# Kernel optimization log

Measured on AMD Instinct MI355X. Metric: run time of the kernel, lower is better.

## Reference

```python
import jax, jax.numpy as jnp
import numpy as np

DIM = 2048
HQ = 32
HKV = 8
HD = DIM // HQ  # 64
B, T = 2, 2048


def _rope_tables(key_unused):
    # Standard RoPE tables: cos/sin of shape [B, T, HD]
    inv_freq = 1.0 / (10000.0 ** (np.arange(0, HD, 2, dtype=np.float32) / HD))
    t = np.arange(T, dtype=np.float32)
    freqs = np.outer(t, inv_freq)                 # [T, HD/2]
    emb = np.concatenate([freqs, freqs], axis=-1)  # [T, HD]
    cos = jnp.asarray(np.cos(emb))[None].repeat(B, axis=0)
    sin = jnp.asarray(np.sin(emb))[None].repeat(B, axis=0)
    return cos, sin


def setup_inputs() -> dict:
    key = jax.random.key(0)
    ks = jax.random.split(key, 8)
    s_in = 1.0 / np.sqrt(DIM)
    x = jax.random.normal(ks[0], (B, T, DIM), dtype=jnp.float32)
    cos, sin = _rope_tables(None)
    # Linear weights stored as [in, out] (transposed vs torch)
    Wq = jax.random.normal(ks[1], (DIM, HQ * HD), dtype=jnp.float32) * s_in
    bq = jnp.zeros((HQ * HD,), dtype=jnp.float32)
    Wk = jax.random.normal(ks[2], (DIM, HKV * HD), dtype=jnp.float32) * s_in
    bk = jnp.zeros((HKV * HD,), dtype=jnp.float32)
    Wv = jax.random.normal(ks[3], (DIM, HKV * HD), dtype=jnp.float32) * s_in
    bv = jnp.zeros((HKV * HD,), dtype=jnp.float32)
    Wo = jax.random.normal(ks[4], (HQ * HD, DIM), dtype=jnp.float32) * s_in
    return {"x": x, "cos": cos, "sin": sin, "Wq": Wq, "bq": bq,
            "Wk": Wk, "bk": bk, "Wv": Wv, "bv": bv, "Wo": Wo}


def _rotate_half(u):
    u1, u2 = jnp.split(u, 2, axis=-1)
    return jnp.concatenate([-u2, u1], axis=-1)


def reference(x, cos, sin, Wq, bq, Wk, bk, Wv, bv, Wo):
    Bx, Tx, D = x.shape
    g = HQ // HKV  # group size (queries per kv head)
    q = (x @ Wq + bq).reshape(Bx, Tx, HQ, HD).transpose(0, 2, 1, 3)   # [B,Hq,T,d]
    k = (x @ Wk + bk).reshape(Bx, Tx, HKV, HD).transpose(0, 2, 1, 3)  # [B,Hkv,T,d]
    v = (x @ Wv + bv).reshape(Bx, Tx, HKV, HD).transpose(0, 2, 1, 3)
    c = cos[:, None, :, :]  # [B,1,T,d]
    s = sin[:, None, :, :]
    q = q * c + _rotate_half(q) * s
    k = k * c + _rotate_half(k) * s
    # GQA: group query heads over shared KV heads instead of repeat_interleave
    qg = q.reshape(Bx, HKV, g, Tx, HD)
    scale = 1.0 / np.sqrt(HD)
    scores = jnp.einsum('bkgtd,bksd->bkgts', qg, k) * scale  # [B,Hkv,g,T,T]
    causal = jnp.tril(jnp.ones((Tx, Tx), dtype=bool))
    scores = jnp.where(causal, scores, jnp.finfo(scores.dtype).min)
    probs = jax.nn.softmax(scores, axis=-1)
    out = jnp.einsum('bkgts,bksd->bkgtd', probs, v)           # [B,Hkv,g,T,d]
    out = out.reshape(Bx, HQ, Tx, HD).transpose(0, 2, 1, 3).reshape(Bx, Tx, HQ * HD)
    return out @ Wo
```

## Files before the change

kernel.cpp:

```cpp
#include <hip/hip_runtime.h>


typedef short s8v __attribute__((ext_vector_type(8)));
typedef float f4v __attribute__((ext_vector_type(4)));

__device__ __forceinline__ unsigned short f2bf(float f) {
  unsigned int u = __float_as_uint(f);
  u += 0x7fffu + ((u >> 16) & 1u);
  return (unsigned short)(u >> 16);
}

__device__ __forceinline__ void llds16(const void* g, void* l) {
  __builtin_amdgcn_global_load_lds(
      (__attribute__((address_space(1))) void*)(g),
      (__attribute__((address_space(3))) void*)(l), 16, 0, 0);
}


__global__ __launch_bounds__(256) void cvt_bf16_k(const float* __restrict__ src,
                                                  unsigned short* __restrict__ dst, int n4) {
  int i = blockIdx.x * blockDim.x + threadIdx.x;
  if (i < n4) {
    float4 v = ((const float4*)src)[i];
    ushort4 o;
    o.x = f2bf(v.x); o.y = f2bf(v.y); o.z = f2bf(v.z); o.w = f2bf(v.w);
    ((ushort4*)dst)[i] = o;
  }
}

__global__ __launch_bounds__(256) void transpose_cvt(const float* __restrict__ src,
                                                     unsigned short* __restrict__ dst,
                                                     int srcW, int K) {
  __shared__ float tile[32][33];
  const int tx = threadIdx.x, ty = threadIdx.y;
  const int x = blockIdx.x * 32 + tx;
  const int ybase = blockIdx.y * 32;
#pragma unroll
  for (int j = 0; j < 32; j += 8)
    tile[ty + j][tx] = src[(size_t)(ybase + ty + j) * srcW + x];
  __syncthreads();
  const int x2 = ybase + tx;
  const int y2 = blockIdx.x * 32 + ty;
#pragma unroll
  for (int j = 0; j < 32; j += 8)
    dst[(size_t)(y2 + j) * K + x2] = f2bf(tile[tx][ty + j]);
}

__device__ __forceinline__ void gemm128(const unsigned short* __restrict__ A,
                                        const unsigned short* __restrict__ Bt,
                                        int K, int m0, int n0,
                                        unsigned short* As, unsigned short* Bs,
                                        f4v acc[4][4]) {
  const int tid = threadIdx.x;
  const int lane = tid & 63;
  const int w = tid >> 6;
  const int wm = w >> 1, wn = w & 1;
  const int c = lane & 15, quad = lane >> 4;
  const int srow = tid >> 2, scol = (tid & 3) * 8;
  for (int k0 = 0; k0 < K; k0 += 32) {
    const unsigned short* ga = A + (size_t)(m0 + srow) * K + k0 + scol;
    const unsigned short* gb = Bt + (size_t)(n0 + srow) * K + k0 + scol;
    llds16(ga,          As + w * 512);
    llds16(ga + 64 * K, As + 2048 + w * 512);
    llds16(gb,          Bs + w * 512);
    llds16(gb + 64 * K, Bs + 2048 + w * 512);
    __syncthreads();
    s8v a[4], b[4];
#pragma unroll
    for (int i = 0; i < 4; ++i)
      a[i] = *(const s8v*)&As[(wm * 64 + i * 16 + c) * 32 + quad * 8];
#pragma unroll
    for (int i = 0; i < 4; ++i)
      b[i] = *(const s8v*)&Bs[(wn * 64 + i * 16 + c) * 32 + quad * 8];
#pragma unroll
    for (int mb = 0; mb < 4; ++mb)
#pragma unroll
      for (int nb = 0; nb < 4; ++nb)
        acc[mb][nb] = __builtin_amdgcn_mfma_f32_16x16x32_bf16(a[mb], b[nb], acc[mb][nb], 0, 0, 0);
    __syncthreads();
  }
}

__global__ __launch_bounds__(256) void gemm_qkv(const unsigned short* __restrict__ A,
    const unsigned short* __restrict__ Bt,
    const float* __restrict__ bq, const float* __restrict__ bk, const float* __restrict__ bv,
    const float* __restrict__ cosp, const float* __restrict__ sinp,
    unsigned short* __restrict__ Qb, unsigned short* __restrict__ Kb,
    unsigned short* __restrict__ Vt) {
  __shared__ unsigned short As[4096], Bs[4096];
  const f4v fzero = {0.f, 0.f, 0.f, 0.f};
  f4v acc[4][4];
#pragma unroll
  for (int i = 0; i < 4; ++i)
#pragma unroll
    for (int j = 0; j < 4; ++j) acc[i][j] = fzero;
  const int m0 = blockIdx.y * 128, n0 = blockIdx.x * 128;
  gemm128(A, Bt, 2048, m0, n0, As, Bs, acc);

  const int tid = threadIdx.x, lane = tid & 63, w = tid >> 6;
  const int wm = w >> 1, wn = w & 1, c = lane & 15, quad = lane >> 4;
  const int nbase = n0 + wn * 64;
#pragma unroll
  for (int mb = 0; mb < 4; ++mb) {
#pragma unroll
    for (int r = 0; r < 4; ++r) {
      const int row = m0 + wm * 64 + mb * 16 + quad * 4 + r;
      const int b = row >> 11, t = row & 2047;
      if (nbase < 2048) {
        const int h = nbase >> 6;
        const size_t ob = ((size_t)(b * 32 + h) * 2048 + t) * 64;
        const float* cb = cosp + (size_t)row * 64;
        const float* sb = sinp + (size_t)row * 64;
#pragma unroll
        for (int nb = 0; nb < 2; ++nb) {
          const int d0 = nb * 16 + c, d1 = d0 + 32;
          const float v0 = acc[mb][nb][r] + bq[nbase + d0];
          const float v1 = acc[mb][nb + 2][r] + bq[nbase + d1];
          Qb[ob + d0] = f2bf(v0 * cb[d0] - v1 * sb[d0]);
          Qb[ob + d1] = f2bf(v1 * cb[d1] + v0 * sb[d1]);
        }
      } else if (nbase < 2560) {
        const int h = (nbase - 2048) >> 6;
        const size_t ob = ((size_t)(b * 8 + h) * 2048 + t) * 64;
        const float* cb = cosp + (size_t)row * 64;
        const float* sb = sinp + (size_t)row * 64;
#pragma unroll
        for (int nb = 0; nb < 2; ++nb) {
          const int d0 = nb * 16 + c, d1 = d0 + 32;
          const float v0 = acc[mb][nb][r] + bk[nbase - 2048 + d0];
          const float v1 = acc[mb][nb + 2][r] + bk[nbase - 2048 + d1];
          Kb[ob + d0] = f2bf(v0 * cb[d0] - v1 * sb[d0]);
          Kb[ob + d1] = f2bf(v1 * cb[d1] + v0 * sb[d1]);
        }
      } else {
        const int h = (nbase - 2560) >> 6;
        const size_t vb = (size_t)(b * 8 + h) * 64;
        const int tl = t & 63;
        const int tp = (t & ~63) | (((tl & 15) << 2) | (tl >> 4));
#pragma unroll
        for (int nb = 0; nb < 4; ++nb) {
          const int d = nb * 16 + c;
          Vt[(vb + d) * 2048 + tp] = f2bf(acc[mb][nb][r] + bv[nbase - 2560 + d]);
        }
      }
    }
  }
}

__global__ __launch_bounds__(256) void attn_k(const unsigned short* __restrict__ Qb,
                                              const unsigned short* __restrict__ Kb,
                                              const unsigned short* __restrict__ Vt,
                                              unsigned short* __restrict__ An) {
  __shared__ unsigned short Qs[4096], Ks[4096], Vs[4096], Ps[4096];
  const int tid = threadIdx.x, lane = tid & 63, w = tid >> 6;
  const int c = lane & 15, quad = lane >> 4;
  const int bh = blockIdx.y;
  const int b = bh >> 5, h = bh & 31, kvh = h >> 2;
  const int qt = gridDim.x - 1 - blockIdx.x;
  const int q0 = qt * 64;
  const unsigned short* gQ = Qb + ((size_t)bh * 2048 + q0) * 64;
  const unsigned short* gK = Kb + (size_t)(b * 8 + kvh) * 2048 * 64;
  const unsigned short* gV = Vt + (size_t)(b * 8 + kvh) * 64 * 2048;

  const int r0 = tid >> 3;
  const int ch8 = (((tid & 7) ^ (r0 & 7))) * 8;

  llds16(gQ + r0 * 64 + ch8,        Qs + w * 512);
  llds16(gQ + (r0 + 32) * 64 + ch8, Qs + 2048 + w * 512);
  __syncthreads();

  const int xq0 = (quad ^ (c & 7)) * 8;
  const int xq1 = ((quad + 4) ^ (c & 7)) * 8;
  const s8v aq0 = *(const s8v*)&Qs[(w * 16 + c) * 64 + xq0];
  const s8v aq1 = *(const s8v*)&Qs[(w * 16 + c) * 64 + xq1];

  const f4v fzero = {0.f, 0.f, 0.f, 0.f};
  f4v O[4];
  float lrp[4];
#pragma unroll
  for (int i = 0; i < 4; ++i) { O[i] = fzero; lrp[i] = 0.f; }

  const float kscale = 0.125f * 1.44269504089f;
  const int ntiles = qt + 1;
  for (int it = 0; it < ntiles; ++it) {
    const int s0 = it * 64;
    llds16(gK + (size_t)(s0 + r0) * 64 + ch8,      Ks + w * 512);
    llds16(gK + (size_t)(s0 + r0 + 32) * 64 + ch8, Ks + 2048 + w * 512);
    llds16(gV + (size_t)r0 * 2048 + s0 + ch8,          Vs + w * 512);
    llds16(gV + (size_t)(r0 + 32) * 2048 + s0 + ch8,   Vs + 2048 + w * 512);
    __syncthreads();

    f4v S[4];
#pragma unroll
    for (int nb = 0; nb < 4; ++nb) {
      const s8v bk0 = *(const s8v*)&Ks[(nb * 16 + c) * 64 + xq0];
      const s8v bk1 = *(const s8v*)&Ks[(nb * 16 + c) * 64 + xq1];
      f4v z = fzero;
      z = __builtin_amdgcn_mfma_f32_16x16x32_bf16(aq0, bk0, z, 0, 0, 0);
      z = __builtin_amdgcn_mfma_f32_16x16x32_bf16(aq1, bk1, z, 0, 0, 0);
      S[nb] = z;
    }

    const bool diag = (it == qt);
#pragma unroll
    for (int r = 0; r < 4; ++r) {
      const int rloc = quad * 4 + r;
      float p[4];
#pragma unroll
      for (int nb = 0; nb < 4; ++nb) {
        float sv = S[nb][r] * kscale;
        if (diag && (nb * 16 + c > w * 16 + rloc)) sv = -1e30f;
        p[nb] = __builtin_amdgcn_exp2f(sv);
      }
      lrp[r] += (p[0] + p[1]) + (p[2] + p[3]);
      ushort4 pk;
      pk.x = f2bf(p[0]); pk.y = f2bf(p[1]); pk.z = f2bf(p[2]); pk.w = f2bf(p[3]);
      *(ushort4*)&Ps[w * 1024 + rloc * 64 + (((c >> 1) ^ (rloc & 7)) * 8) + (c & 1) * 4] = pk;
    }
    asm volatile("s_waitcnt lgkmcnt(0)" ::: "memory");

    const s8v ap0 = *(const s8v*)&Ps[w * 1024 + c * 64 + xq0];
    const s8v ap1 = *(const s8v*)&Ps[w * 1024 + c * 64 + xq1];
#pragma unroll
    for (int nbd = 0; nbd < 4; ++nbd) {
      const s8v bv0 = *(const s8v*)&Vs[(nbd * 16 + c) * 64 + xq0];
      const s8v bv1 = *(const s8v*)&Vs[(nbd * 16 + c) * 64 + xq1];
      O[nbd] = __builtin_amdgcn_mfma_f32_16x16x32_bf16(ap0, bv0, O[nbd], 0, 0, 0);
      O[nbd] = __builtin_amdgcn_mfma_f32_16x16x32_bf16(ap1, bv1, O[nbd], 0, 0, 0);
    }
    __syncthreads();
  }

#pragma unroll
  for (int r = 0; r < 4; ++r) {
    float ps = lrp[r];
    ps += __shfl_xor(ps, 1, 64);
    ps += __shfl_xor(ps, 2, 64);
    ps += __shfl_xor(ps, 4, 64);
    ps += __shfl_xor(ps, 8, 64);
    const float inv = 1.0f / ps;
    const int t = q0 + w * 16 + quad * 4 + r;
    const size_t rowb = ((size_t)b * 2048 + t) * 2048 + h * 64;
#pragma unroll
    for (int nbd = 0; nbd < 4; ++nbd)
      An[rowb + nbd * 16 + c] = f2bf(O[nbd][r] * inv);
  }
}

__global__ __launch_bounds__(256) void gemm_out(const unsigned short* __restrict__ A,
                                                const unsigned short* __restrict__ Bt,
                                                float* __restrict__ C) {
  __shared__ unsigned short As[4096], Bs[4096];
  const f4v fzero = {0.f, 0.f, 0.f, 0.f};
  f4v acc[4][4];
#pragma unroll
  for (int i = 0; i < 4; ++i)
#pragma unroll
    for (int j = 0; j < 4; ++j) acc[i][j] = fzero;
  const int m0 = blockIdx.y * 128, n0 = blockIdx.x * 128;
  gemm128(A, Bt, 2048, m0, n0, As, Bs, acc);
  const int tid = threadIdx.x, lane = tid & 63, w = tid >> 6;
  const int wm = w >> 1, wn = w & 1, c = lane & 15, quad = lane >> 4;
#pragma unroll
  for (int mb = 0; mb < 4; ++mb)
#pragma unroll
    for (int r = 0; r < 4; ++r) {
      const int row = m0 + wm * 64 + mb * 16 + quad * 4 + r;
#pragma unroll
      for (int nb = 0; nb < 4; ++nb)
        C[(size_t)row * 2048 + n0 + wn * 64 + nb * 16 + c] = acc[mb][nb][r];
    }
}

extern "C" void kernel_launch(void* const* d_in, const int* in_sizes, int n_in,
                              void* d_out, int out_size, void* d_ws, size_t ws_size,
                              hipStream_t stream) {
  const float* x    = (const float*)d_in[0];
  const float* cosp = (const float*)d_in[1];
  const float* sinp = (const float*)d_in[2];
  const float* Wq   = (const float*)d_in[3];
  const float* bq   = (const float*)d_in[4];
  const float* Wk   = (const float*)d_in[5];
  const float* bk   = (const float*)d_in[6];
  const float* Wv   = (const float*)d_in[7];
  const float* bv   = (const float*)d_in[8];
  const float* Wo   = (const float*)d_in[9];
  float* out = (float*)d_out;

  char* ws = (char*)d_ws;
  unsigned short* xb  = (unsigned short*)(ws);
  unsigned short* Wt  = (unsigned short*)(ws + 16777216);
  unsigned short* Wot = (unsigned short*)(ws + 29360128);
  unsigned short* Qb  = (unsigned short*)(ws + 37748736);
  unsigned short* Kb  = (unsigned short*)(ws + 54525952);
  unsigned short* Vt  = (unsigned short*)(ws + 58720256);
  unsigned short* An  = (unsigned short*)(ws + 62914560);

  cvt_bf16_k<<<8192, 256, 0, stream>>>(x, xb, 2097152);
  dim3 tb(32, 8);
  transpose_cvt<<<dim3(64, 64), tb, 0, stream>>>(Wq, Wt, 2048, 2048);
  transpose_cvt<<<dim3(16, 64), tb, 0, stream>>>(Wk, Wt + (size_t)2048 * 2048, 512, 2048);
  transpose_cvt<<<dim3(16, 64), tb, 0, stream>>>(Wv, Wt + (size_t)2560 * 2048, 512, 2048);
  transpose_cvt<<<dim3(64, 64), tb, 0, stream>>>(Wo, Wot, 2048, 2048);
  gemm_qkv<<<dim3(24, 32), 256, 0, stream>>>(xb, Wt, bq, bk, bv, cosp, sinp, Qb, Kb, Vt);
  attn_k<<<dim3(32, 64), 256, 0, stream>>>(Qb, Kb, Vt, An);
  gemm_out<<<dim3(16, 32), 256, 0, stream>>>(An, Wot, out);
}
```

Before: 398.5 us.

## Fuse prep kernels, swizzle GEMM LDS, double-buffer attention K/V, fold scale into Q

Merges the five conversion and transpose launches into a single prep kernel, which removes launch overhead. Adds an XOR swizzle to the GEMM shared-memory tiles to cut bank conflicts. Folds the softmax scale and log2e factor into Q during the QKV epilogue. Double-buffers the K/V tiles in attention so the next tile's loads overlap compute, reusing the Q buffer for P. Uses packed bf16 conversion for P. The attention loop's top barrier is gone, so correctness depends on the remaining end-of-loop sync and on the async LDS loads completing in time.

```diff
diff --git a/kernel.cpp b/kernel.cpp
--- a/kernel.cpp
+++ b/kernel.cpp
@@ -10,40 +10,55 @@
   return (unsigned short)(u >> 16);
 }
 
+__device__ __forceinline__ unsigned int pk_bf16(float a, float b) {
+#if __has_builtin(__builtin_amdgcn_cvt_pk_bf16_f32)
+  auto r = __builtin_amdgcn_cvt_pk_bf16_f32(a, b);
+  return *(unsigned int*)&r;
+#else
+  return (unsigned int)f2bf(a) | ((unsigned int)f2bf(b) << 16);
+#endif
+}
+
 __device__ __forceinline__ void llds16(const void* g, void* l) {
   __builtin_amdgcn_global_load_lds(
       (__attribute__((address_space(1))) void*)(g),
       (__attribute__((address_space(3))) void*)(l), 16, 0, 0);
 }
 
-
-__global__ __launch_bounds__(256) void cvt_bf16_k(const float* __restrict__ src,
-                                                  unsigned short* __restrict__ dst, int n4) {
-  int i = blockIdx.x * blockDim.x + threadIdx.x;
-  if (i < n4) {
-    float4 v = ((const float4*)src)[i];
+__global__ __launch_bounds__(256) void prep_k(const float* __restrict__ x,
+    const float* __restrict__ Wq, const float* __restrict__ Wk,
+    const float* __restrict__ Wv, const float* __restrict__ Wo,
+    unsigned short* __restrict__ xb, unsigned short* __restrict__ Wt,
+    unsigned short* __restrict__ Wot) {
+  const int tid = threadIdx.x;
+  int bid = blockIdx.x;
+  if (bid < 8192) {
+    const int i = bid * 256 + tid;
+    float4 v = ((const float4*)x)[i];
     ushort4 o;
     o.x = f2bf(v.x); o.y = f2bf(v.y); o.z = f2bf(v.z); o.w = f2bf(v.w);
-    ((ushort4*)dst)[i] = o;
-  }
-}
-
-__global__ __launch_bounds__(256) void transpose_cvt(const float* __restrict__ src,
-                                                     unsigned short* __restrict__ dst,
-                                                     int srcW, int K) {
+    ((ushort4*)xb)[i] = o;
+    return;
+  }
+  bid -= 8192;
+  const float* src; unsigned short* dst; int srcW, bx, by;
+  if (bid < 4096)      { src = Wq; dst = Wt;                        srcW = 2048; bx = bid & 63;        by = bid >> 6; }
+  else if (bid < 5120) { src = Wk; dst = Wt + (size_t)2048 * 2048;  srcW = 512;  bx = (bid - 4096) & 15; by = (bid - 4096) >> 4; }
+  else if (bid < 6144) { src = Wv; dst = Wt + (size_t)2560 * 2048;  srcW = 512;  bx = (bid - 5120) & 15; by = (bid - 5120) >> 4; }
+  else                 { src = Wo; dst = Wot;                       srcW = 2048; bx = (bid - 6144) & 63; by = (bid - 6144) >> 6; }
   __shared__ float tile[32][33];
-  const int tx = threadIdx.x, ty = threadIdx.y;
-  const int x = blockIdx.x * 32 + tx;
-  const int ybase = blockIdx.y * 32;
+  const int tx = tid & 31, ty = tid >> 5;
+  const int xg = bx * 32 + tx;
+  const int ybase = by * 32;
 #pragma unroll
   for (int j = 0; j < 32; j += 8)
-    tile[ty + j][tx] = src[(size_t)(ybase + ty + j) * srcW + x];
+    tile[ty + j][tx] = src[(size_t)(ybase + ty + j) * srcW + xg];
   __syncthreads();
   const int x2 = ybase + tx;
-  const int y2 = blockIdx.x * 32 + ty;
+  const int y2 = bx * 32 + ty;
 #pragma unroll
   for (int j = 0; j < 32; j += 8)
-    dst[(size_t)(y2 + j) * K + x2] = f2bf(tile[tx][ty + j]);
+    dst[(size_t)(y2 + j) * 2048 + x2] = f2bf(tile[tx][ty + j]);
 }
 
 __device__ __forceinline__ void gemm128(const unsigned short* __restrict__ A,
@@ -56,7 +71,9 @@
   const int w = tid >> 6;
   const int wm = w >> 1, wn = w & 1;
   const int c = lane & 15, quad = lane >> 4;
-  const int srow = tid >> 2, scol = (tid & 3) * 8;
+  const int srow = tid >> 2;
+  const int scol = ((tid & 3) ^ ((tid >> 3) & 3)) * 8;
+  const int ca = (quad ^ ((c >> 1) & 3)) * 8;
   for (int k0 = 0; k0 < K; k0 += 32) {
     const unsigned short* ga = A + (size_t)(m0 + srow) * K + k0 + scol;
     const unsigned short* gb = Bt + (size_t)(n0 + srow) * K + k0 + scol;
@@ -68,10 +85,10 @@
     s8v a[4], b[4];
 #pragma unroll
     for (int i = 0; i < 4; ++i)
-      a[i] = *(const s8v*)&As[(wm * 64 + i * 16 + c) * 32 + quad * 8];
+      a[i] = *(const s8v*)&As[(wm * 64 + i * 16 + c) * 32 + ca];
 #pragma unroll
     for (int i = 0; i < 4; ++i)
-      b[i] = *(const s8v*)&Bs[(wn * 64 + i * 16 + c) * 32 + quad * 8];
+      b[i] = *(const s8v*)&Bs[(wn * 64 + i * 16 + c) * 32 + ca];
 #pragma unroll
     for (int mb = 0; mb < 4; ++mb)
 #pragma unroll
@@ -100,6 +117,7 @@
   const int tid = threadIdx.x, lane = tid & 63, w = tid >> 6;
   const int wm = w >> 1, wn = w & 1, c = lane & 15, quad = lane >> 4;
   const int nbase = n0 + wn * 64;
+  const float QSC = 0.125f * 1.44269504089f;
 #pragma unroll
   for (int mb = 0; mb < 4; ++mb) {
 #pragma unroll
@@ -116,8 +134,8 @@
           const int d0 = nb * 16 + c, d1 = d0 + 32;
           const float v0 = acc[mb][nb][r] + bq[nbase + d0];
           const float v1 = acc[mb][nb + 2][r] + bq[nbase + d1];
-          Qb[ob + d0] = f2bf(v0 * cb[d0] - v1 * sb[d0]);
-          Qb[ob + d1] = f2bf(v1 * cb[d1] + v0 * sb[d1]);
+          Qb[ob + d0] = f2bf((v0 * cb[d0] - v1 * sb[d0]) * QSC);
+          Qb[ob + d1] = f2bf((v1 * cb[d1] + v0 * sb[d1]) * QSC);
         }
       } else if (nbase < 2560) {
         const int h = (nbase - 2048) >> 6;
@@ -151,7 +169,8 @@
                                               const unsigned short* __restrict__ Kb,
                                               const unsigned short* __restrict__ Vt,
                                               unsigned short* __restrict__ An) {
-  __shared__ unsigned short Qs[4096], Ks[4096], Vs[4096], Ps[4096];
+  __shared__ unsigned short QPs[4096];
+  __shared__ unsigned short Ks[2][4096], Vs[2][4096];
   const int tid = threadIdx.x, lane = tid & 63, w = tid >> 6;
   const int c = lane & 15, quad = lane >> 4;
   const int bh = blockIdx.y;
@@ -163,16 +182,20 @@
   const unsigned short* gV = Vt + (size_t)(b * 8 + kvh) * 64 * 2048;
 
   const int r0 = tid >> 3;
-  const int ch8 = (((tid & 7) ^ (r0 & 7))) * 8;
-
-  llds16(gQ + r0 * 64 + ch8,        Qs + w * 512);
-  llds16(gQ + (r0 + 32) * 64 + ch8, Qs + 2048 + w * 512);
+  const int ch8 = ((tid & 7) ^ (r0 & 7)) * 8;
+
+  llds16(gQ + r0 * 64 + ch8,        QPs + w * 512);
+  llds16(gQ + (r0 + 32) * 64 + ch8, QPs + 2048 + w * 512);
+  llds16(gK + r0 * 64 + ch8,        Ks[0] + w * 512);
+  llds16(gK + (r0 + 32) * 64 + ch8, Ks[0] + 2048 + w * 512);
+  llds16(gV + (size_t)r0 * 2048 + ch8,        Vs[0] + w * 512);
+  llds16(gV + (size_t)(r0 + 32) * 2048 + ch8, Vs[0] + 2048 + w * 512);
   __syncthreads();
 
   const int xq0 = (quad ^ (c & 7)) * 8;
   const int xq1 = ((quad + 4) ^ (c & 7)) * 8;
-  const s8v aq0 = *(const s8v*)&Qs[(w * 16 + c) * 64 + xq0];
-  const s8v aq1 = *(const s8v*)&Qs[(w * 16 + c) * 64 + xq1];
+  const s8v aq0 = *(const s8v*)&QPs[(w * 16 + c) * 64 + xq0];
+  const s8v aq1 = *(const s8v*)&QPs[(w * 16 + c) * 64 + xq1];
 
   const f4v fzero = {0.f, 0.f, 0.f, 0.f};
   f4v O[4];
@@ -180,21 +203,22 @@
 #pragma unroll
   for (int i = 0; i < 4; ++i) { O[i] = fzero; lrp[i] = 0.f; }
 
-  const float kscale = 0.125f * 1.44269504089f;
   const int ntiles = qt + 1;
   for (int it = 0; it < ntiles; ++it) {
-    const int s0 = it * 64;
-    llds16(gK + (size_t)(s0 + r0) * 64 + ch8,      Ks + w * 512);
-    llds16(gK + (size_t)(s0 + r0 + 32) * 64 + ch8, Ks + 2048 + w * 512);
-    llds16(gV + (size_t)r0 * 2048 + s0 + ch8,          Vs + w * 512);
-    llds16(gV + (size_t)(r0 + 32) * 2048 + s0 + ch8,   Vs + 2048 + w * 512);
-    __syncthreads();
+    const int cur = it & 1;
+    if (it + 1 < ntiles) {
+      const int s1 = (it + 1) * 64, nxt = cur ^ 1;
+      llds16(gK + (size_t)(s1 + r0) * 64 + ch8,      Ks[nxt] + w * 512);
+      llds16(gK + (size_t)(s1 + r0 + 32) * 64 + ch8, Ks[nxt] + 2048 + w * 512);
+      llds16(gV + (size_t)r0 * 2048 + s1 + ch8,        Vs[nxt] + w * 512);
+      llds16(gV + (size_t)(r0 + 32) * 2048 + s1 + ch8, Vs[nxt] + 2048 + w * 512);
+    }
 
     f4v S[4];
 #pragma unroll
     for (int nb = 0; nb < 4; ++nb) {
-      const s8v bk0 = *(const s8v*)&Ks[(nb * 16 + c) * 64 + xq0];
-      const s8v bk1 = *(const s8v*)&Ks[(nb * 16 + c) * 64 + xq1];
+      const s8v bk0 = *(const s8v*)&Ks[cur][(nb * 16 + c) * 64 + xq0];
+      const s8v bk1 = *(const s8v*)&Ks[cur][(nb * 16 + c) * 64 + xq1];
       f4v z = fzero;
       z = __builtin_amdgcn_mfma_f32_16x16x32_bf16(aq0, bk0, z, 0, 0, 0);
       z = __builtin_amdgcn_mfma_f32_16x16x32_bf16(aq1, bk1, z, 0, 0, 0);
@@ -208,23 +232,24 @@
       float p[4];
 #pragma unroll
       for (int nb = 0; nb < 4; ++nb) {
-        float sv = S[nb][r] * kscale;
+        float sv = S[nb][r];
         if (diag && (nb * 16 + c > w * 16 + rloc)) sv = -1e30f;
         p[nb] = __builtin_amdgcn_exp2f(sv);
       }
       lrp[r] += (p[0] + p[1]) + (p[2] + p[3]);
-      ushort4 pk;
-      pk.x = f2bf(p[0]); pk.y = f2bf(p[1]); pk.z = f2bf(p[2]); pk.w = f2bf(p[3]);
-      *(ushort4*)&Ps[w * 1024 + rloc * 64 + (((c >> 1) ^ (rloc & 7)) * 8) + (c & 1) * 4] = pk;
+      uint2 pk2;
+      pk2.x = pk_bf16(p[0], p[1]);
+      pk2.y = pk_bf16(p[2], p[3]);
+      *(uint2*)&QPs[w * 1024 + rloc * 64 + (((c >> 1) ^ (rloc & 7)) * 8) + (c & 1) * 4] = pk2;
     }
     asm volatile("s_waitcnt lgkmcnt(0)" ::: "memory");
 
-    const s8v ap0 = *(const s8v*)&Ps[w * 1024 + c * 64 + xq0];
-    const s8v ap1 = *(const s8v*)&Ps[w * 1024 + c * 64 + xq1];
+    const s8v ap0 = *(const s8v*)&QPs[w * 1024 + c * 64 + xq0];
+    const s8v ap1 = *(const s8v*)&QPs[w * 1024 + c * 64 + xq1];
 #pragma unroll
     for (int nbd = 0; nbd < 4; ++nbd) {
-      const s8v bv0 = *(const s8v*)&Vs[(nbd * 16 + c) * 64 + xq0];
-      const s8v bv1 = *(const s8v*)&Vs[(nbd * 16 + c) * 64 + xq1];
+      const s8v bv0 = *(const s8v*)&Vs[cur][(nbd * 16 + c) * 64 + xq0];
+      const s8v bv1 = *(const s8v*)&Vs[cur][(nbd * 16 + c) * 64 + xq1];
       O[nbd] = __builtin_amdgcn_mfma_f32_16x16x32_bf16(ap0, bv0, O[nbd], 0, 0, 0);
       O[nbd] = __builtin_amdgcn_mfma_f32_16x16x32_bf16(ap1, bv1, O[nbd], 0, 0, 0);
     }
@@ -296,12 +321,7 @@
   unsigned short* Vt  = (unsigned short*)(ws + 58720256);
   unsigned short* An  = (unsigned short*)(ws + 62914560);
 
-  cvt_bf16_k<<<8192, 256, 0, stream>>>(x, xb, 2097152);
-  dim3 tb(32, 8);
-  transpose_cvt<<<dim3(64, 64), tb, 0, stream>>>(Wq, Wt, 2048, 2048);
-  transpose_cvt<<<dim3(16, 64), tb, 0, stream>>>(Wk, Wt + (size_t)2048 * 2048, 512, 2048);
-  transpose_cvt<<<dim3(16, 64), tb, 0, stream>>>(Wv, Wt + (size_t)2560 * 2048, 512, 2048);
-  transpose_cvt<<<dim3(64, 64), tb, 0, stream>>>(Wo, Wot, 2048, 2048);
+  prep_k<<<18432, 256, 0, stream>>>(x, Wq, Wk, Wv, Wo, xb, Wt, Wot);
   gemm_qkv<<<dim3(24, 32), 256, 0, stream>>>(xb, Wt, bq, bk, bv, cosp, sinp, Qb, Kb, Vt);
   attn_k<<<dim3(32, 64), 256, 0, stream>>>(Qb, Kb, Vt, An);
   gemm_out<<<dim3(16, 32), 256, 0, stream>>>(An, Wot, out);
```

Result: faster. 379.2 us (-4.9%).
